# Kernel tuning notes

Measured on AMD Instinct MI355X. Metric: run time of the kernel, lower is better.

The kernel has to match this reference:

```python
import jax, jax.numpy as jnp
import numpy as np


def setup_inputs() -> dict:
    key = jax.random.key(0)
    k1, k2 = jax.random.split(key)
    b, c, h, w = 8, 256, 96, 192
    x = jax.random.normal(k1, (b, c, h, w), dtype=jnp.float32)
    y = jax.random.normal(k2, (b, c, h, w), dtype=jnp.float32)
    return {"x": x, "y": y, "max_displacement": 4}


def _correlation(x, y, md):
    # x, y: [B, C, H, W]. Output: [B, K*K, H, W], K = 2*md+1.
    b, c, h, w = x.shape
    K = 2 * md + 1
    # zero-pad y spatially so out-of-bounds displacements contribute 0
    yp = jnp.pad(y, ((0, 0), (0, 0), (md, md), (md, md)))
    # fixed small loop over K*K displacements (81 for md=4)
    outs = [
        jnp.einsum('bchw,bchw->bhw', x, yp[:, :, di:di + h, dj:dj + w])
        for di in range(K) for dj in range(K)
    ]
    out = jnp.stack(outs, axis=1)  # [B, K*K, H, W]
    return out / c


def reference(x, y, max_displacement):
    return _correlation(x, y, max_displacement)
```

## Files before the change

kernel.cpp:

```cpp
#include <hip/hip_runtime.h>
#include <hip/hip_bf16.h>
#include <stdint.h>


using f32x4 = __attribute__((ext_vector_type(4))) float;
using s16x4 = __attribute__((ext_vector_type(4))) short;
using u16x4 = __attribute__((ext_vector_type(4))) unsigned short;

#define C_DIM 256
#define H_DIM 96
#define W_DIM 192
#define HWSZ  (H_DIM * W_DIM)
#define MD 4
#define KD 9
#define CHUNK 32
#define NCHUNK 8
#define NTHR 512
#define WTILES 12
#define HQ 24
#define SUB_B 128
#define YROW_B (16 * SUB_B)
#define NROWS 12
#define BUFSZ (NROWS * YROW_B)
#define LDS_BYTES (2 * BUFSZ)
#define NYQ (NROWS * CHUNK * 6)

static __device__ __forceinline__ unsigned short bf16b(float f) {
  __bf16 h = (__bf16)f;
  unsigned short s; __builtin_memcpy(&s, &h, 2); return s;
}

static __device__ __forceinline__ s16x4 tr16(uint32_t addr) {
  s16x4 d;
  asm volatile("ds_read_b64_tr_b16 %0, %1" : "=v"(d) : "v"(addr));
  return d;
}

#define WAITLG(n) asm volatile("s_waitcnt lgkmcnt(" #n ")" ::: "memory")

__global__ __launch_bounds__(NTHR, 4)
void corr_mfma(const float* __restrict__ xg, const float* __restrict__ yg,
               float* __restrict__ outg) {
  __shared__ __align__(16) char smem[LDS_BYTES];

  const int bid = blockIdx.x;
  const int b   = bid & 7;
  const int rem = bid >> 3;
  const int wt  = rem / HQ;
  const int hq  = rem - wt * HQ;
  const int w0  = wt * 16;
  const int h0  = hq * 4;

  const int tid  = threadIdx.x;
  const int lane = tid & 63;
  const int wv   = tid >> 6;
  const int hh   = wv & 3;
  const int dh   = wv >> 2;
  const int hi   = lane >> 4;
  const int lm   = lane & 15;

  const uint32_t sbase = (uint32_t)(uintptr_t)&smem[0];

  uint32_t goffY[5], loffY[5];
  uint32_t vmY = 0, exY = 0;
#pragma unroll
  for (int i = 0; i < 5; ++i) {
    const int qid = i * NTHR + tid;
    goffY[i] = 0u; loffY[i] = 0u;
    if (qid < NYQ) {
      exY |= (1u << i);
      const int q = qid % 6;
      const int c = (qid / 6) & 31;
      const int r = qid / 192;
      const int hg = h0 + r - MD;
      const int sg = w0 - MD + 4 * q;
      const bool ok = (hg >= 0) && (hg < H_DIM) && (sg >= 0) && (sg < W_DIM);
      if (ok) vmY |= (1u << i);
      goffY[i] = ok ? (uint32_t)(((b * C_DIM + c) * H_DIM + hg) * W_DIM + sg) : 0u;
      const int s = 4 * q;
      loffY[i] = r * YROW_B + (s >> 4) * 1024 + (c >> 2) * SUB_B + (c & 3) * 32 + (s & 15) * 2;
    }
  }

  const int h = h0 + hh;
  uint32_t xoff[8];
#pragma unroll
  for (int e = 0; e < 8; ++e) {
    const int ce = (e < 4) ? (hi * 4 + e) : (16 + hi * 4 + (e - 4));
    xoff[e] = (uint32_t)(((b * C_DIM + ce) * H_DIM + h) * W_DIM + w0 + lm);
  }

  f32x4 acc[5][2];
#pragma unroll
  for (int dl = 0; dl < 5; ++dl) {
    acc[dl][0] = f32x4{0.f, 0.f, 0.f, 0.f};
    acc[dl][1] = f32x4{0.f, 0.f, 0.f, 0.f};
  }

  const uint32_t bbase = sbase + (uint32_t)(hh + dh * 4) * YROW_B + hi * SUB_B + lm * 8;

  float4 yv[5];
  float  xv[8];
  s16x4  afr0, afr1;

  {
#pragma unroll
    for (int i = 0; i < 5; ++i) {
      float4 t4 = make_float4(0.f, 0.f, 0.f, 0.f);
      if (vmY & (1u << i)) t4 = *(const float4*)(yg + goffY[i]);
      yv[i] = t4;
    }
#pragma unroll
    for (int e = 0; e < 8; ++e) xv[e] = xg[xoff[e]];
#pragma unroll
    for (int i = 0; i < 5; ++i)
      if (exY & (1u << i))
        *(u16x4*)(smem + loffY[i]) =
            u16x4{bf16b(yv[i].x), bf16b(yv[i].y), bf16b(yv[i].z), bf16b(yv[i].w)};
    afr0[0] = (short)bf16b(xv[0]); afr0[1] = (short)bf16b(xv[1]);
    afr0[2] = (short)bf16b(xv[2]); afr0[3] = (short)bf16b(xv[3]);
    afr1[0] = (short)bf16b(xv[4]); afr1[1] = (short)bf16b(xv[5]);
    afr1[2] = (short)bf16b(xv[6]); afr1[3] = (short)bf16b(xv[7]);
    const uint32_t co = (uint32_t)CHUNK * HWSZ;
#pragma unroll
    for (int i = 0; i < 5; ++i) {
      float4 t4 = make_float4(0.f, 0.f, 0.f, 0.f);
      if (vmY & (1u << i)) t4 = *(const float4*)(yg + goffY[i] + co);
      yv[i] = t4;
    }
#pragma unroll
    for (int e = 0; e < 8; ++e) xv[e] = xg[xoff[e] + co];
  }
  __syncthreads();

  for (int t = 0; t < NCHUNK; ++t) {
    const uint32_t bo = (uint32_t)(t & 1) * BUFSZ;
    s16x4 bsl[2][4];

#define ISSUE_DL(dl) { \
    const uint32_t ba = bbase + bo + (uint32_t)(dl) * YROW_B; \
    bsl[(dl) & 1][0] = tr16(ba);               \
    bsl[(dl) & 1][1] = tr16(ba + 512);         \
    bsl[(dl) & 1][2] = tr16(ba + 1024);        \
    bsl[(dl) & 1][3] = tr16(ba + 1536); }

#define DO_DL(dl, lg) \
    WAITLG(lg); __builtin_amdgcn_sched_barrier(0); \
    acc[dl][0] = __builtin_amdgcn_mfma_f32_16x16x16bf16_1k(afr0, bsl[(dl) & 1][0], acc[dl][0], 0, 0, 0); \
    acc[dl][0] = __builtin_amdgcn_mfma_f32_16x16x16bf16_1k(afr1, bsl[(dl) & 1][1], acc[dl][0], 0, 0, 0); \
    acc[dl][1] = __builtin_amdgcn_mfma_f32_16x16x16bf16_1k(afr0, bsl[(dl) & 1][2], acc[dl][1], 0, 0, 0); \
    acc[dl][1] = __builtin_amdgcn_mfma_f32_16x16x16bf16_1k(afr1, bsl[(dl) & 1][3], acc[dl][1], 0, 0, 0);

    __builtin_amdgcn_s_setprio(1);
    ISSUE_DL(0)
    ISSUE_DL(1)
    DO_DL(0, 4)
    ISSUE_DL(2)
    DO_DL(1, 4)
    ISSUE_DL(3)
    DO_DL(2, 4)
    ISSUE_DL(4)
    DO_DL(3, 4)
    DO_DL(4, 0)
    __builtin_amdgcn_s_setprio(0);
#undef ISSUE_DL
#undef DO_DL

    if (t + 1 < NCHUNK) {
      const uint32_t wo = (uint32_t)((t + 1) & 1) * BUFSZ;
#pragma unroll
      for (int i = 0; i < 5; ++i)
        if (exY & (1u << i))
          *(u16x4*)(smem + wo + loffY[i]) =
              u16x4{bf16b(yv[i].x), bf16b(yv[i].y), bf16b(yv[i].z), bf16b(yv[i].w)};
      afr0[0] = (short)bf16b(xv[0]); afr0[1] = (short)bf16b(xv[1]);
      afr0[2] = (short)bf16b(xv[2]); afr0[3] = (short)bf16b(xv[3]);
      afr1[0] = (short)bf16b(xv[4]); afr1[1] = (short)bf16b(xv[5]);
      afr1[2] = (short)bf16b(xv[6]); afr1[3] = (short)bf16b(xv[7]);
      if (t + 2 < NCHUNK) {
        const uint32_t co = (uint32_t)(t + 2) * CHUNK * HWSZ;
#pragma unroll
        for (int i = 0; i < 5; ++i) {
          float4 t4 = make_float4(0.f, 0.f, 0.f, 0.f);
          if (vmY & (1u << i)) t4 = *(const float4*)(yg + goffY[i] + co);
          yv[i] = t4;
        }
#pragma unroll
        for (int e = 0; e < 8; ++e) xv[e] = xg[xoff[e] + co];
      }
    }
    __syncthreads();
  }

  const float scale = 1.f / 256.f;
#pragma unroll
  for (int dl = 0; dl < 5; ++dl) {
    const int di = dh * 4 + dl;
#pragma unroll
    for (int tt = 0; tt < 2; ++tt) {
#pragma unroll
      for (int rg = 0; rg < 4; ++rg) {
        const int m = hi * 4 + rg;
        const int dj = tt * 16 + lm - m;
        if (0 <= dj && dj <= 8) {
          outg[((b * (KD * KD) + di * KD + dj) * H_DIM + h) * W_DIM + w0 + m] =
              acc[dl][tt][rg] * scale;
        }
      }
    }
  }
}

extern "C" void kernel_launch(void* const* d_in, const int* in_sizes, int n_in,
                              void* d_out, int out_size, void* d_ws, size_t ws_size,
                              hipStream_t stream) {
  const float* x = (const float*)d_in[0];
  const float* y = (const float*)d_in[1];
  float* out = (float*)d_out;
  (void)in_sizes; (void)n_in; (void)d_ws; (void)ws_size; (void)out_size;

  const int grid = 8 * HQ * WTILES;
  corr_mfma<<<dim3(grid), dim3(NTHR), 0, stream>>>(x, y, out);
}
```

Measured before the change: 153.4 us.

## Give each wave a full 9-row displacement set over an 8-row tile

Each block now covers 8 output rows instead of 4, with each of the 8 waves handling one output row and all 9 vertical displacements, rather than two waves splitting the displacements. The y halo tile grows from 12 to 16 rows, so the staged-row overhead per output row drops and the grid shrinks by half. Global prefetch is now issued at the start of each chunk iteration instead of two chunks ahead. The cost is more accumulator registers per wave (18 f32x4), fewer blocks to fill the GPU, and a shorter prefetch distance.

```diff
diff --git a/kernel.cpp b/kernel.cpp
--- a/kernel.cpp
+++ b/kernel.cpp
@@ -17,10 +17,10 @@
 #define NCHUNK 8
 #define NTHR 512
 #define WTILES 12
-#define HQ 24
+#define HQ 12
 #define SUB_B 128
 #define YROW_B (16 * SUB_B)
-#define NROWS 12
+#define NROWS 16
 #define BUFSZ (NROWS * YROW_B)
 #define LDS_BYTES (2 * BUFSZ)
 #define NYQ (NROWS * CHUNK * 6)
@@ -49,40 +49,34 @@
   const int wt  = rem / HQ;
   const int hq  = rem - wt * HQ;
   const int w0  = wt * 16;
-  const int h0  = hq * 4;
+  const int h0  = hq * 8;
 
   const int tid  = threadIdx.x;
   const int lane = tid & 63;
   const int wv   = tid >> 6;
-  const int hh   = wv & 3;
-  const int dh   = wv >> 2;
   const int hi   = lane >> 4;
   const int lm   = lane & 15;
 
   const uint32_t sbase = (uint32_t)(uintptr_t)&smem[0];
 
-  uint32_t goffY[5], loffY[5];
-  uint32_t vmY = 0, exY = 0;
-#pragma unroll
-  for (int i = 0; i < 5; ++i) {
+  uint32_t goffY[6], loffY[6];
+  uint32_t vmY = 0;
+#pragma unroll
+  for (int i = 0; i < 6; ++i) {
     const int qid = i * NTHR + tid;
-    goffY[i] = 0u; loffY[i] = 0u;
-    if (qid < NYQ) {
-      exY |= (1u << i);
-      const int q = qid % 6;
-      const int c = (qid / 6) & 31;
-      const int r = qid / 192;
-      const int hg = h0 + r - MD;
-      const int sg = w0 - MD + 4 * q;
-      const bool ok = (hg >= 0) && (hg < H_DIM) && (sg >= 0) && (sg < W_DIM);
-      if (ok) vmY |= (1u << i);
-      goffY[i] = ok ? (uint32_t)(((b * C_DIM + c) * H_DIM + hg) * W_DIM + sg) : 0u;
-      const int s = 4 * q;
-      loffY[i] = r * YROW_B + (s >> 4) * 1024 + (c >> 2) * SUB_B + (c & 3) * 32 + (s & 15) * 2;
-    }
-  }
-
-  const int h = h0 + hh;
+    const int q = qid % 6;
+    const int c = (qid / 6) & 31;
+    const int r = qid / 192;
+    const int hg = h0 + r - MD;
+    const int sg = w0 - MD + 4 * q;
+    const bool ok = (hg >= 0) && (hg < H_DIM) && (sg >= 0) && (sg < W_DIM);
+    if (ok) vmY |= (1u << i);
+    goffY[i] = ok ? (uint32_t)(((b * C_DIM + c) * H_DIM + hg) * W_DIM + sg) : 0u;
+    const int s = 4 * q;
+    loffY[i] = r * YROW_B + (s >> 4) * 1024 + (c >> 2) * SUB_B + (c & 3) * 32 + (s & 15) * 2;
+  }
+
+  const int h = h0 + wv;
   uint32_t xoff[8];
 #pragma unroll
   for (int e = 0; e < 8; ++e) {
@@ -90,22 +84,22 @@
     xoff[e] = (uint32_t)(((b * C_DIM + ce) * H_DIM + h) * W_DIM + w0 + lm);
   }
 
-  f32x4 acc[5][2];
-#pragma unroll
-  for (int dl = 0; dl < 5; ++dl) {
-    acc[dl][0] = f32x4{0.f, 0.f, 0.f, 0.f};
-    acc[dl][1] = f32x4{0.f, 0.f, 0.f, 0.f};
-  }
-
-  const uint32_t bbase = sbase + (uint32_t)(hh + dh * 4) * YROW_B + hi * SUB_B + lm * 8;
-
-  float4 yv[5];
+  f32x4 acc[KD][2];
+#pragma unroll
+  for (int di = 0; di < KD; ++di) {
+    acc[di][0] = f32x4{0.f, 0.f, 0.f, 0.f};
+    acc[di][1] = f32x4{0.f, 0.f, 0.f, 0.f};
+  }
+
+  const uint32_t bbase = sbase + (uint32_t)wv * YROW_B + hi * SUB_B + lm * 8;
+
+  float4 yv[6];
   float  xv[8];
   s16x4  afr0, afr1;
 
   {
 #pragma unroll
-    for (int i = 0; i < 5; ++i) {
+    for (int i = 0; i < 6; ++i) {
       float4 t4 = make_float4(0.f, 0.f, 0.f, 0.f);
       if (vmY & (1u << i)) t4 = *(const float4*)(yg + goffY[i]);
       yv[i] = t4;
@@ -113,89 +107,86 @@
 #pragma unroll
     for (int e = 0; e < 8; ++e) xv[e] = xg[xoff[e]];
 #pragma unroll
-    for (int i = 0; i < 5; ++i)
-      if (exY & (1u << i))
-        *(u16x4*)(smem + loffY[i]) =
-            u16x4{bf16b(yv[i].x), bf16b(yv[i].y), bf16b(yv[i].z), bf16b(yv[i].w)};
+    for (int i = 0; i < 6; ++i)
+      *(u16x4*)(smem + loffY[i]) =
+          u16x4{bf16b(yv[i].x), bf16b(yv[i].y), bf16b(yv[i].z), bf16b(yv[i].w)};
     afr0[0] = (short)bf16b(xv[0]); afr0[1] = (short)bf16b(xv[1]);
     afr0[2] = (short)bf16b(xv[2]); afr0[3] = (short)bf16b(xv[3]);
     afr1[0] = (short)bf16b(xv[4]); afr1[1] = (short)bf16b(xv[5]);
     afr1[2] = (short)bf16b(xv[6]); afr1[3] = (short)bf16b(xv[7]);
-    const uint32_t co = (uint32_t)CHUNK * HWSZ;
-#pragma unroll
-    for (int i = 0; i < 5; ++i) {
-      float4 t4 = make_float4(0.f, 0.f, 0.f, 0.f);
-      if (vmY & (1u << i)) t4 = *(const float4*)(yg + goffY[i] + co);
-      yv[i] = t4;
-    }
-#pragma unroll
-    for (int e = 0; e < 8; ++e) xv[e] = xg[xoff[e] + co];
   }
   __syncthreads();
 
   for (int t = 0; t < NCHUNK; ++t) {
+    if (t + 1 < NCHUNK) {
+      const uint32_t co = (uint32_t)(t + 1) * CHUNK * HWSZ;
+#pragma unroll
+      for (int i = 0; i < 6; ++i) {
+        float4 t4 = make_float4(0.f, 0.f, 0.f, 0.f);
+        if (vmY & (1u << i)) t4 = *(const float4*)(yg + goffY[i] + co);
+        yv[i] = t4;
+      }
+#pragma unroll
+      for (int e = 0; e < 8; ++e) xv[e] = xg[xoff[e] + co];
+    }
+
     const uint32_t bo = (uint32_t)(t & 1) * BUFSZ;
     s16x4 bsl[2][4];
 
-#define ISSUE_DL(dl) { \
-    const uint32_t ba = bbase + bo + (uint32_t)(dl) * YROW_B; \
-    bsl[(dl) & 1][0] = tr16(ba);               \
-    bsl[(dl) & 1][1] = tr16(ba + 512);         \
-    bsl[(dl) & 1][2] = tr16(ba + 1024);        \
-    bsl[(dl) & 1][3] = tr16(ba + 1536); }
-
-#define DO_DL(dl, lg) \
+#define ISSUE_DI(di) { \
+    const uint32_t ba = bbase + bo + (uint32_t)(di) * YROW_B; \
+    bsl[(di) & 1][0] = tr16(ba);           \
+    bsl[(di) & 1][1] = tr16(ba + 512);     \
+    bsl[(di) & 1][2] = tr16(ba + 1024);    \
+    bsl[(di) & 1][3] = tr16(ba + 1536); }
+
+#define DO_DI(di, lg) \
     WAITLG(lg); __builtin_amdgcn_sched_barrier(0); \
-    acc[dl][0] = __builtin_amdgcn_mfma_f32_16x16x16bf16_1k(afr0, bsl[(dl) & 1][0], acc[dl][0], 0, 0, 0); \
-    acc[dl][0] = __builtin_amdgcn_mfma_f32_16x16x16bf16_1k(afr1, bsl[(dl) & 1][1], acc[dl][0], 0, 0, 0); \
-    acc[dl][1] = __builtin_amdgcn_mfma_f32_16x16x16bf16_1k(afr0, bsl[(dl) & 1][2], acc[dl][1], 0, 0, 0); \
-    acc[dl][1] = __builtin_amdgcn_mfma_f32_16x16x16bf16_1k(afr1, bsl[(dl) & 1][3], acc[dl][1], 0, 0, 0);
+    acc[di][0] = __builtin_amdgcn_mfma_f32_16x16x16bf16_1k(afr0, bsl[(di) & 1][0], acc[di][0], 0, 0, 0); \
+    acc[di][0] = __builtin_amdgcn_mfma_f32_16x16x16bf16_1k(afr1, bsl[(di) & 1][1], acc[di][0], 0, 0, 0); \
+    acc[di][1] = __builtin_amdgcn_mfma_f32_16x16x16bf16_1k(afr0, bsl[(di) & 1][2], acc[di][1], 0, 0, 0); \
+    acc[di][1] = __builtin_amdgcn_mfma_f32_16x16x16bf16_1k(afr1, bsl[(di) & 1][3], acc[di][1], 0, 0, 0);
 
     __builtin_amdgcn_s_setprio(1);
-    ISSUE_DL(0)
-    ISSUE_DL(1)
-    DO_DL(0, 4)
-    ISSUE_DL(2)
-    DO_DL(1, 4)
-    ISSUE_DL(3)
-    DO_DL(2, 4)
-    ISSUE_DL(4)
-    DO_DL(3, 4)
-    DO_DL(4, 0)
+    ISSUE_DI(0)
+    ISSUE_DI(1)
+    DO_DI(0, 4)
+    ISSUE_DI(2)
+    DO_DI(1, 4)
+    ISSUE_DI(3)
+    DO_DI(2, 4)
+    ISSUE_DI(4)
+    DO_DI(3, 4)
+    ISSUE_DI(5)
+    DO_DI(4, 4)
+    ISSUE_DI(6)
+    DO_DI(5, 4)
+    ISSUE_DI(7)
+    DO_DI(6, 4)
+    ISSUE_DI(8)
+    DO_DI(7, 4)
+    DO_DI(8, 0)
     __builtin_amdgcn_s_setprio(0);
-#undef ISSUE_DL
-#undef DO_DL
+#undef ISSUE_DI
+#undef DO_DI
 
     if (t + 1 < NCHUNK) {
       const uint32_t wo = (uint32_t)((t + 1) & 1) * BUFSZ;
 #pragma unroll
-      for (int i = 0; i < 5; ++i)
-        if (exY & (1u << i))
-          *(u16x4*)(smem + wo + loffY[i]) =
-              u16x4{bf16b(yv[i].x), bf16b(yv[i].y), bf16b(yv[i].z), bf16b(yv[i].w)};
+      for (int i = 0; i < 6; ++i)
+        *(u16x4*)(smem + wo + loffY[i]) =
+            u16x4{bf16b(yv[i].x), bf16b(yv[i].y), bf16b(yv[i].z), bf16b(yv[i].w)};
       afr0[0] = (short)bf16b(xv[0]); afr0[1] = (short)bf16b(xv[1]);
       afr0[2] = (short)bf16b(xv[2]); afr0[3] = (short)bf16b(xv[3]);
       afr1[0] = (short)bf16b(xv[4]); afr1[1] = (short)bf16b(xv[5]);
       afr1[2] = (short)bf16b(xv[6]); afr1[3] = (short)bf16b(xv[7]);
-      if (t + 2 < NCHUNK) {
-        const uint32_t co = (uint32_t)(t + 2) * CHUNK * HWSZ;
-#pragma unroll
-        for (int i = 0; i < 5; ++i) {
-          float4 t4 = make_float4(0.f, 0.f, 0.f, 0.f);
-          if (vmY & (1u << i)) t4 = *(const float4*)(yg + goffY[i] + co);
-          yv[i] = t4;
-        }
-#pragma unroll
-        for (int e = 0; e < 8; ++e) xv[e] = xg[xoff[e] + co];
-      }
     }
     __syncthreads();
   }
 
   const float scale = 1.f / 256.f;
 #pragma unroll
-  for (int dl = 0; dl < 5; ++dl) {
-    const int di = dh * 4 + dl;
+  for (int di = 0; di < KD; ++di) {
 #pragma unroll
     for (int tt = 0; tt < 2; ++tt) {
 #pragma unroll
@@ -204,7 +195,7 @@
         const int dj = tt * 16 + lm - m;
         if (0 <= dj && dj <= 8) {
           outg[((b * (KD * KD) + di * KD + dj) * H_DIM + h) * W_DIM + w0 + m] =
-              acc[dl][tt][rg] * scale;
+              acc[di][tt][rg] * scale;
         }
       }
     }
```

After: 202.6 us. +32.1%, slower.

## Split displacement rows across blocks with eight output rows per block

Applied to the files above, without the earlier changes.

Work is repartitioned so each block covers 8 output rows and 3 vertical displacements, with one row per wave, instead of 4 rows split across two overlapping groups of 5 displacements. This removes the duplicate computation of the middle displacement row and lowers per-block LDS footprint so 5 blocks can fit per CU. In exchange the grid grows and each x tile is reloaded by three blocks, raising global and L2 traffic. The register prefetch is also shortened from two chunks ahead to one, issued at the top of each iteration.

```diff
diff --git a/kernel.cpp b/kernel.cpp
--- a/kernel.cpp
+++ b/kernel.cpp
@@ -13,14 +13,15 @@
 #define HWSZ  (H_DIM * W_DIM)
 #define MD 4
 #define KD 9
+#define NDG 3
 #define CHUNK 32
 #define NCHUNK 8
 #define NTHR 512
 #define WTILES 12
-#define HQ 24
+#define HQ 12
 #define SUB_B 128
 #define YROW_B (16 * SUB_B)
-#define NROWS 12
+#define NROWS 10
 #define BUFSZ (NROWS * YROW_B)
 #define LDS_BYTES (2 * BUFSZ)
 #define NYQ (NROWS * CHUNK * 6)
@@ -38,33 +39,34 @@
 
 #define WAITLG(n) asm volatile("s_waitcnt lgkmcnt(" #n ")" ::: "memory")
 
-__global__ __launch_bounds__(NTHR, 4)
+__global__ __launch_bounds__(NTHR, 5)
 void corr_mfma(const float* __restrict__ xg, const float* __restrict__ yg,
                float* __restrict__ outg) {
   __shared__ __align__(16) char smem[LDS_BYTES];
 
   const int bid = blockIdx.x;
   const int b   = bid & 7;
-  const int rem = bid >> 3;
-  const int wt  = rem / HQ;
-  const int hq  = rem - wt * HQ;
+  const int r2  = bid >> 3;
+  const int dg  = r2 % NDG;
+  const int r3  = r2 / NDG;
+  const int hq  = r3 % HQ;
+  const int wt  = r3 / HQ;
   const int w0  = wt * 16;
-  const int h0  = hq * 4;
+  const int h0  = hq * 8;
+  const int yr0 = h0 - MD + dg * NDG;
 
   const int tid  = threadIdx.x;
   const int lane = tid & 63;
   const int wv   = tid >> 6;
-  const int hh   = wv & 3;
-  const int dh   = wv >> 2;
   const int hi   = lane >> 4;
   const int lm   = lane & 15;
 
   const uint32_t sbase = (uint32_t)(uintptr_t)&smem[0];
 
-  uint32_t goffY[5], loffY[5];
+  uint32_t goffY[4], loffY[4];
   uint32_t vmY = 0, exY = 0;
 #pragma unroll
-  for (int i = 0; i < 5; ++i) {
+  for (int i = 0; i < 4; ++i) {
     const int qid = i * NTHR + tid;
     goffY[i] = 0u; loffY[i] = 0u;
     if (qid < NYQ) {
@@ -72,7 +74,7 @@
       const int q = qid % 6;
       const int c = (qid / 6) & 31;
       const int r = qid / 192;
-      const int hg = h0 + r - MD;
+      const int hg = yr0 + r;
       const int sg = w0 - MD + 4 * q;
       const bool ok = (hg >= 0) && (hg < H_DIM) && (sg >= 0) && (sg < W_DIM);
       if (ok) vmY |= (1u << i);
@@ -82,7 +84,7 @@
     }
   }
 
-  const int h = h0 + hh;
+  const int h = h0 + wv;
   uint32_t xoff[8];
 #pragma unroll
   for (int e = 0; e < 8; ++e) {
@@ -90,22 +92,22 @@
     xoff[e] = (uint32_t)(((b * C_DIM + ce) * H_DIM + h) * W_DIM + w0 + lm);
   }
 
-  f32x4 acc[5][2];
-#pragma unroll
-  for (int dl = 0; dl < 5; ++dl) {
+  f32x4 acc[NDG][2];
+#pragma unroll
+  for (int dl = 0; dl < NDG; ++dl) {
     acc[dl][0] = f32x4{0.f, 0.f, 0.f, 0.f};
     acc[dl][1] = f32x4{0.f, 0.f, 0.f, 0.f};
   }
 
-  const uint32_t bbase = sbase + (uint32_t)(hh + dh * 4) * YROW_B + hi * SUB_B + lm * 8;
-
-  float4 yv[5];
+  const uint32_t bbase = sbase + (uint32_t)wv * YROW_B + hi * SUB_B + lm * 8;
+
+  float4 yv[4];
   float  xv[8];
   s16x4  afr0, afr1;
 
   {
 #pragma unroll
-    for (int i = 0; i < 5; ++i) {
+    for (int i = 0; i < 4; ++i) {
       float4 t4 = make_float4(0.f, 0.f, 0.f, 0.f);
       if (vmY & (1u << i)) t4 = *(const float4*)(yg + goffY[i]);
       yv[i] = t4;
@@ -113,7 +115,7 @@
 #pragma unroll
     for (int e = 0; e < 8; ++e) xv[e] = xg[xoff[e]];
 #pragma unroll
-    for (int i = 0; i < 5; ++i)
+    for (int i = 0; i < 4; ++i)
       if (exY & (1u << i))
         *(u16x4*)(smem + loffY[i]) =
             u16x4{bf16b(yv[i].x), bf16b(yv[i].y), bf16b(yv[i].z), bf16b(yv[i].w)};
@@ -121,27 +123,30 @@
     afr0[2] = (short)bf16b(xv[2]); afr0[3] = (short)bf16b(xv[3]);
     afr1[0] = (short)bf16b(xv[4]); afr1[1] = (short)bf16b(xv[5]);
     afr1[2] = (short)bf16b(xv[6]); afr1[3] = (short)bf16b(xv[7]);
-    const uint32_t co = (uint32_t)CHUNK * HWSZ;
-#pragma unroll
-    for (int i = 0; i < 5; ++i) {
-      float4 t4 = make_float4(0.f, 0.f, 0.f, 0.f);
-      if (vmY & (1u << i)) t4 = *(const float4*)(yg + goffY[i] + co);
-      yv[i] = t4;
-    }
-#pragma unroll
-    for (int e = 0; e < 8; ++e) xv[e] = xg[xoff[e] + co];
   }
   __syncthreads();
 
   for (int t = 0; t < NCHUNK; ++t) {
+    if (t + 1 < NCHUNK) {
+      const uint32_t co = (uint32_t)(t + 1) * CHUNK * HWSZ;
+#pragma unroll
+      for (int i = 0; i < 4; ++i) {
+        float4 t4 = make_float4(0.f, 0.f, 0.f, 0.f);
+        if (vmY & (1u << i)) t4 = *(const float4*)(yg + goffY[i] + co);
+        yv[i] = t4;
+      }
+#pragma unroll
+      for (int e = 0; e < 8; ++e) xv[e] = xg[xoff[e] + co];
+    }
+
     const uint32_t bo = (uint32_t)(t & 1) * BUFSZ;
     s16x4 bsl[2][4];
 
 #define ISSUE_DL(dl) { \
     const uint32_t ba = bbase + bo + (uint32_t)(dl) * YROW_B; \
-    bsl[(dl) & 1][0] = tr16(ba);               \
-    bsl[(dl) & 1][1] = tr16(ba + 512);         \
-    bsl[(dl) & 1][2] = tr16(ba + 1024);        \
+    bsl[(dl) & 1][0] = tr16(ba);           \
+    bsl[(dl) & 1][1] = tr16(ba + 512);     \
+    bsl[(dl) & 1][2] = tr16(ba + 1024);    \
     bsl[(dl) & 1][3] = tr16(ba + 1536); }
 
 #define DO_DL(dl, lg) \
@@ -157,11 +162,7 @@
     DO_DL(0, 4)
     ISSUE_DL(2)
     DO_DL(1, 4)
-    ISSUE_DL(3)
-    DO_DL(2, 4)
-    ISSUE_DL(4)
-    DO_DL(3, 4)
-    DO_DL(4, 0)
+    DO_DL(2, 0)
     __builtin_amdgcn_s_setprio(0);
 #undef ISSUE_DL
 #undef DO_DL
@@ -169,7 +170,7 @@
     if (t + 1 < NCHUNK) {
       const uint32_t wo = (uint32_t)((t + 1) & 1) * BUFSZ;
 #pragma unroll
-      for (int i = 0; i < 5; ++i)
+      for (int i = 0; i < 4; ++i)
         if (exY & (1u << i))
           *(u16x4*)(smem + wo + loffY[i]) =
               u16x4{bf16b(yv[i].x), bf16b(yv[i].y), bf16b(yv[i].z), bf16b(yv[i].w)};
@@ -177,25 +178,14 @@
       afr0[2] = (short)bf16b(xv[2]); afr0[3] = (short)bf16b(xv[3]);
       afr1[0] = (short)bf16b(xv[4]); afr1[1] = (short)bf16b(xv[5]);
       afr1[2] = (short)bf16b(xv[6]); afr1[3] = (short)bf16b(xv[7]);
-      if (t + 2 < NCHUNK) {
-        const uint32_t co = (uint32_t)(t + 2) * CHUNK * HWSZ;
-#pragma unroll
-        for (int i = 0; i < 5; ++i) {
-          float4 t4 = make_float4(0.f, 0.f, 0.f, 0.f);
-          if (vmY & (1u << i)) t4 = *(const float4*)(yg + goffY[i] + co);
-          yv[i] = t4;
-        }
-#pragma unroll
-        for (int e = 0; e < 8; ++e) xv[e] = xg[xoff[e] + co];
-      }
     }
     __syncthreads();
   }
 
   const float scale = 1.f / 256.f;
 #pragma unroll
-  for (int dl = 0; dl < 5; ++dl) {
-    const int di = dh * 4 + dl;
+  for (int dl = 0; dl < NDG; ++dl) {
+    const int di = dg * NDG + dl;
 #pragma unroll
     for (int tt = 0; tt < 2; ++tt) {
 #pragma unroll
@@ -219,6 +209,6 @@
   float* out = (float*)d_out;
   (void)in_sizes; (void)n_in; (void)d_ws; (void)ws_size; (void)out_size;
 
-  const int grid = 8 * HQ * WTILES;
+  const int grid = WTILES * HQ * NDG * 8;
   corr_mfma<<<dim3(grid), dim3(NTHR), 0, stream>>>(x, y, out);
 }
```

Measured after the change: 262.2 us. 70.9% more time.
